# Optimization experiments

Measured on AMD Instinct MI355X. Metric: run time of the kernel, lower is better.

## Reference

```python
import jax, jax.numpy as jnp
import numpy as np

N = 50000
E = 800000
EPS = 1e-5


def layer_norm(h, g, b):
    m = jnp.mean(h, axis=-1, keepdims=True)
    v = jnp.mean((h - m) ** 2, axis=-1, keepdims=True)
    return (h - m) * jax.lax.rsqrt(v + EPS) * g + b


def gcn_conv(x, src, dst, w, W, b):
    # PyG GCNConv: add self-loops (weight 1), symmetric normalization,
    # linear transform, scatter-add aggregation at dst, plus bias.
    n = x.shape[0]
    loop = jnp.arange(n)
    s = jnp.concatenate([src, loop])
    d = jnp.concatenate([dst, loop])
    wf = jnp.concatenate([w, jnp.ones((n,), dtype=x.dtype)])
    deg = jax.ops.segment_sum(wf, d, num_segments=n)
    dinv = jnp.where(deg > 0, deg, 1.0) ** -0.5
    dinv = jnp.where(deg > 0, dinv, 0.0)
    norm = dinv[s] * wf * dinv[d]            # [E+N]
    h = x @ W                                 # [N, out]
    msg = h[s] * norm[:, None]                # gather + scale
    out = jax.ops.segment_sum(msg, d, num_segments=n)  # scatter-add
    return out + b


def setup_inputs() -> dict:
    key = jax.random.key(0)
    ks = jax.random.split(key, 16)
    din, dh, dout = 128, 128, 64
    p = lambda k, shp: jax.random.normal(k, shp, dtype=jnp.float32) * 0.05
    return {
        "x": jax.random.normal(ks[0], (N, din), dtype=jnp.float32),
        "edge_index": jax.random.randint(ks[1], (2, E), 0, N),
        "edge_weight": jax.random.uniform(ks[2], (E,), dtype=jnp.float32),
        "W1": p(ks[3], (din, dh)), "b1": jnp.zeros((dh,), jnp.float32),
        "g1": jnp.ones((dh,), jnp.float32), "t1": jnp.zeros((dh,), jnp.float32),
        "W2": p(ks[4], (dh, dh)), "b2": jnp.zeros((dh,), jnp.float32),
        "g2": jnp.ones((dh,), jnp.float32), "t2": jnp.zeros((dh,), jnp.float32),
        "W3": p(ks[5], (dh, dout)), "b3": jnp.zeros((dout,), jnp.float32),
        "g3": jnp.ones((dout,), jnp.float32), "t3": jnp.zeros((dout,), jnp.float32),
    }


def reference(x, edge_index, edge_weight, W1, b1, g1, t1, W2, b2, g2, t2, W3, b3, g3, t3):
    src, dst = edge_index[0], edge_index[1]
    h = gcn_conv(x, src, dst, edge_weight, W1, b1)
    h = jax.nn.relu(layer_norm(h, g1, t1))
    h = gcn_conv(h, src, dst, edge_weight, W2, b2)
    h = jax.nn.relu(layer_norm(h, g2, t2))
    h = gcn_conv(h, src, dst, edge_weight, W3, b3)
    h = layer_norm(h, g3, t3)  # last layer: no relu/dropout
    return h
```

## Files before the change

kernel.cpp:

```cpp
#include <hip/hip_runtime.h>


typedef __attribute__((ext_vector_type(8))) short short8;
typedef __attribute__((ext_vector_type(4))) float f32x4;

static constexpr float FXS  = 16777216.0f;
static constexpr float FXSI = 1.0f / 16777216.0f;

__device__ __forceinline__ unsigned short f2bf(float f) {
    unsigned int u = __float_as_uint(f);
    u += 0x7FFFu + ((u >> 16) & 1u);
    return (unsigned short)(u >> 16);
}

__global__ __launch_bounds__(256) void edge_pass_kernel(
    const int* __restrict__ dst, const float* __restrict__ ew,
    unsigned long long* __restrict__ packed, int* __restrict__ rank, int nE)
{
    int e = blockIdx.x * 256 + threadIdx.x;
    if (e >= nE) return;
    const int d = dst[e];
    const unsigned long long fx = (unsigned long long)__float2uint_rn(ew[e] * FXS);
    const unsigned long long old = atomicAdd(&packed[d], (1ULL << 40) | fx);
    rank[e] = (int)(old >> 40);
}

__global__ __launch_bounds__(256) void dinv_partial_kernel(
    const unsigned long long* __restrict__ packed, int* __restrict__ partials,
    float* __restrict__ dinv, int n)
{
    const int b = blockIdx.x;
    const int i = b * 256 + threadIdx.x;
    int c = 0;
    if (i < n) {
        const unsigned long long p = packed[i];
        c = (int)(p >> 40);
        const float deg = (float)(p & ((1ULL << 40) - 1)) * FXSI;
        dinv[i] = rsqrtf(deg + 1.0f);
    }
#pragma unroll
    for (int off = 32; off; off >>= 1) c += __shfl_xor(c, off);
    __shared__ int red[4];
    if ((threadIdx.x & 63) == 0) red[threadIdx.x >> 6] = c;
    __syncthreads();
    if (threadIdx.x == 0) partials[b] = red[0] + red[1] + red[2] + red[3];
}

__global__ __launch_bounds__(256) void scanp_kernel(
    int* __restrict__ partials, int* __restrict__ rowptr, int n, int nblk)
{
    __shared__ int buf[256];
    const int v = (threadIdx.x < nblk) ? partials[threadIdx.x] : 0;
    buf[threadIdx.x] = v;
    __syncthreads();
    for (int off = 1; off < 256; off <<= 1) {
        const int t = (threadIdx.x >= off) ? buf[threadIdx.x - off] : 0;
        __syncthreads();
        buf[threadIdx.x] += t;
        __syncthreads();
    }
    if (threadIdx.x < nblk) partials[threadIdx.x] = buf[threadIdx.x] - v;
    if (threadIdx.x == 255) rowptr[n] = buf[255];
}

__global__ __launch_bounds__(256) void scanf_kernel(
    const unsigned long long* __restrict__ packed, const int* __restrict__ partials,
    int* __restrict__ rowptr, int n)
{
    __shared__ int buf[256];
    const int b = blockIdx.x;
    const int i = b * 256 + threadIdx.x;
    const int v = (i < n) ? (int)(packed[i] >> 40) : 0;
    buf[threadIdx.x] = v;
    __syncthreads();
    for (int off = 1; off < 256; off <<= 1) {
        const int t = (threadIdx.x >= off) ? buf[threadIdx.x - off] : 0;
        __syncthreads();
        buf[threadIdx.x] += t;
        __syncthreads();
    }
    if (i < n) rowptr[i] = buf[threadIdx.x] - v + partials[b];
}

__global__ __launch_bounds__(256) void fill2_kernel(
    const int* __restrict__ src, const int* __restrict__ dst,
    const float* __restrict__ ew, const int* __restrict__ rank,
    const float* __restrict__ dinv, const int* __restrict__ rowptr,
    int2* __restrict__ edges, int nE)
{
    int e = blockIdx.x * 256 + threadIdx.x;
    if (e >= nE) return;
    const int s = src[e], d = dst[e];
    const float nrm = dinv[s] * ew[e] * dinv[d];
    edges[rowptr[d] + rank[e]] = make_int2(s, __float_as_int(nrm));
}

__global__ __launch_bounds__(256) void xconv_kernel(
    const float* __restrict__ X, unsigned short* __restrict__ Xb, int total4)
{
    int i = blockIdx.x * 256 + threadIdx.x;
    if (i >= total4) return;
    const float4 v = ((const float4*)X)[i];
    ushort4 o;
    o.x = f2bf(v.x); o.y = f2bf(v.y); o.z = f2bf(v.z); o.w = f2bf(v.w);
    ((ushort4*)Xb)[i] = o;
}

__global__ __launch_bounds__(256) void wconv_kernel(
    const float* __restrict__ W1, const float* __restrict__ W2,
    const float* __restrict__ W3, unsigned short* __restrict__ Wt1,
    unsigned short* __restrict__ Wt2, unsigned short* __restrict__ Wt3)
{
    int i = blockIdx.x * 256 + threadIdx.x;
    if (i < 16384) {
        const int j = i >> 7, k = i & 127;
        Wt1[i] = f2bf(W1[k * 128 + j]);
    } else if (i < 32768) {
        const int q = i - 16384, j = q >> 7, k = q & 127;
        Wt2[q] = f2bf(W2[k * 128 + j]);
    } else if (i < 40960) {
        const int q = i - 32768, j = q >> 7, k = q & 127;
        Wt3[q] = f2bf(W3[k * 64 + j]);
    }
}

template<int DOUT>
__global__ __launch_bounds__(256) void gemm_mfma_kernel(
    const unsigned short* __restrict__ Xb,
    const unsigned short* __restrict__ Wt,
    unsigned short* __restrict__ H, int n)
{
    const int wave = threadIdx.x >> 6;
    const int lane = threadIdx.x & 63;
    const int row0 = (blockIdx.x * 4 + wave) * 16;
    if (row0 >= n) return;
    const int lr = lane & 15;
    const int lk = (lane >> 4) * 8;

    constexpr int NCT = DOUT / 16;
    f32x4 acc[NCT];
#pragma unroll
    for (int c = 0; c < NCT; ++c) acc[c] = (f32x4){0.f, 0.f, 0.f, 0.f};

    const int arow = row0 + lr;
    const bool rv = arow < n;
    short8 afrag[4];
#pragma unroll
    for (int ks = 0; ks < 4; ++ks)
        afrag[ks] = rv ? *(const short8*)(Xb + (size_t)arow * 128 + ks * 32 + lk)
                       : (short8){0, 0, 0, 0, 0, 0, 0, 0};

#pragma unroll
    for (int c = 0; c < NCT; ++c) {
        const unsigned short* wp = Wt + (size_t)(c * 16 + lr) * 128 + lk;
#pragma unroll
        for (int ks = 0; ks < 4; ++ks) {
            const short8 bfrag = *(const short8*)(wp + ks * 32);
            acc[c] = __builtin_amdgcn_mfma_f32_16x16x32_bf16(afrag[ks], bfrag, acc[c], 0, 0, 0);
        }
    }

    const int orow0 = row0 + (lane >> 4) * 4;
#pragma unroll
    for (int c = 0; c < NCT; ++c) {
#pragma unroll
        for (int r = 0; r < 4; ++r) {
            const int orow = orow0 + r;
            if (orow < n) H[(size_t)orow * DOUT + c * 16 + lr] = f2bf(acc[c][r]);
        }
    }
}

template<int D, bool RELU, bool OB16>
__global__ __launch_bounds__(256) void gather_ln_kernel(
    const unsigned short* __restrict__ H, const int2* __restrict__ edges,
    const int* __restrict__ rowptr, const float* __restrict__ dinv,
    const float* __restrict__ bias, const float* __restrict__ g,
    const float* __restrict__ t, void* __restrict__ OUT, int n)
{
    constexpr int PL = D / 64;
    const int lane = threadIdx.x & 63;
    const int node = blockIdx.x * 4 + (threadIdx.x >> 6);
    if (node >= n) return;

    const float di = dinv[node];
    const float sn = di * di;
    float acc[PL];
    {
        const unsigned short* hd = H + (size_t)node * D + lane * PL;
        if constexpr (PL == 2) {
            const unsigned int w = *(const unsigned int*)hd;
            acc[0] = fmaf(__uint_as_float(w << 16), sn, bias[lane * 2]);
            acc[1] = fmaf(__uint_as_float(w & 0xFFFF0000u), sn, bias[lane * 2 + 1]);
        } else {
            acc[0] = fmaf(__uint_as_float((unsigned int)hd[0] << 16), sn, bias[lane]);
        }
    }

    const int k0 = rowptr[node], k1 = rowptr[node + 1];
    for (int base = k0; base < k1; base += 64) {
        int2 ed = make_int2(0, 0);
        if (base + lane < k1) ed = edges[base + lane];
        const int cnt = min(64, k1 - base);
        int j = 0;
        for (; j + 4 <= cnt; j += 4) {
#pragma unroll
            for (int u = 0; u < 4; ++u) {
                const int   s   = __shfl(ed.x, j + u);
                const float nrm = __int_as_float(__shfl(ed.y, j + u));
                const unsigned short* hs = H + (size_t)s * D + lane * PL;
                if constexpr (PL == 2) {
                    const unsigned int w = *(const unsigned int*)hs;
                    acc[0] = fmaf(__uint_as_float(w << 16), nrm, acc[0]);
                    acc[1] = fmaf(__uint_as_float(w & 0xFFFF0000u), nrm, acc[1]);
                } else {
                    acc[0] = fmaf(__uint_as_float((unsigned int)hs[0] << 16), nrm, acc[0]);
                }
            }
        }
        for (; j < cnt; ++j) {
            const int   s   = __shfl(ed.x, j);
            const float nrm = __int_as_float(__shfl(ed.y, j));
            const unsigned short* hs = H + (size_t)s * D + lane * PL;
            if constexpr (PL == 2) {
                const unsigned int w = *(const unsigned int*)hs;
                acc[0] = fmaf(__uint_as_float(w << 16), nrm, acc[0]);
                acc[1] = fmaf(__uint_as_float(w & 0xFFFF0000u), nrm, acc[1]);
            } else {
                acc[0] = fmaf(__uint_as_float((unsigned int)hs[0] << 16), nrm, acc[0]);
            }
        }
    }

    float s1 = 0.f;
#pragma unroll
    for (int i = 0; i < PL; ++i) s1 += acc[i];
#pragma unroll
    for (int off = 32; off; off >>= 1) s1 += __shfl_xor(s1, off);
    const float m = s1 * (1.f / D);
    float s2 = 0.f;
#pragma unroll
    for (int i = 0; i < PL; ++i) { acc[i] -= m; s2 += acc[i] * acc[i]; }
#pragma unroll
    for (int off = 32; off; off >>= 1) s2 += __shfl_xor(s2, off);
    const float rs = rsqrtf(s2 * (1.f / D) + 1e-5f);

    float r[PL];
#pragma unroll
    for (int i = 0; i < PL; ++i) {
        r[i] = fmaf(acc[i] * rs, g[lane * PL + i], t[lane * PL + i]);
        if (RELU) r[i] = fmaxf(r[i], 0.f);
    }
    if constexpr (OB16) {
        static_assert(PL == 2, "bf16 output path assumes D=128");
        const unsigned int w = (unsigned int)f2bf(r[0]) | ((unsigned int)f2bf(r[1]) << 16);
        ((unsigned int*)OUT)[(size_t)node * (D / 2) + lane] = w;
    } else {
        float* o = (float*)OUT + (size_t)node * D + lane * PL;
#pragma unroll
        for (int i = 0; i < PL; ++i) o[i] = r[i];
    }
}

extern "C" void kernel_launch(void* const* d_in, const int* in_sizes, int n_in,
                              void* d_out, int out_size, void* d_ws, size_t ws_size,
                              hipStream_t stream)
{
    const float* x  = (const float*)d_in[0];
    const int*   ei = (const int*)  d_in[1];
    const float* ew = (const float*)d_in[2];
    const float* W1 = (const float*)d_in[3];
    const float* b1 = (const float*)d_in[4];
    const float* g1 = (const float*)d_in[5];
    const float* t1 = (const float*)d_in[6];
    const float* W2 = (const float*)d_in[7];
    const float* b2 = (const float*)d_in[8];
    const float* g2 = (const float*)d_in[9];
    const float* t2 = (const float*)d_in[10];
    const float* W3 = (const float*)d_in[11];
    const float* b3 = (const float*)d_in[12];
    const float* g3 = (const float*)d_in[13];
    const float* t3 = (const float*)d_in[14];

    const int n  = in_sizes[0] / 128;
    const int nE = in_sizes[1] / 2;
    const int* srcv = ei;
    const int* dstv = ei + nE;

    const size_t na   = ((size_t)n + 63) & ~(size_t)63;
    const int    nblk = (n + 255) / 256;
    const int    eb   = (nE + 255) / 256;

    unsigned long long* packed = (unsigned long long*)d_ws;
    float* dinv     = (float*)(packed + na);
    int*   rowptr   = (int*)(dinv + na);
    int*   partials = rowptr + na + 64;
    int2*  edges    = (int2*)(partials + 256);
    unsigned short* Hb  = (unsigned short*)(edges + nE);
    unsigned short* Qb  = Hb + (size_t)n * 128;
    unsigned short* xb  = Qb + (size_t)n * 128;
    unsigned short* Wt1 = xb + (size_t)n * 128;
    unsigned short* Wt2 = Wt1 + 16384;
    unsigned short* Wt3 = Wt2 + 16384;
    int* rank = (int*)Hb;

    hipMemsetAsync(packed, 0, na * sizeof(unsigned long long), stream);

    edge_pass_kernel   <<<eb,   256, 0, stream>>>(dstv, ew, packed, rank, nE);
    dinv_partial_kernel<<<nblk, 256, 0, stream>>>(packed, partials, dinv, n);
    scanp_kernel       <<<1,    256, 0, stream>>>(partials, rowptr, n, nblk);
    scanf_kernel       <<<nblk, 256, 0, stream>>>(packed, partials, rowptr, n);
    fill2_kernel       <<<eb,   256, 0, stream>>>(srcv, dstv, ew, rank, dinv, rowptr, edges, nE);

    xconv_kernel<<<(n * 32 + 255) / 256, 256, 0, stream>>>(x, xb, n * 32);
    wconv_kernel<<<160, 256, 0, stream>>>(W1, W2, W3, Wt1, Wt2, Wt3);

    const int gb = (n + 63) / 64;
    const int nb = (n + 3) / 4;

    gemm_mfma_kernel<128><<<gb, 256, 0, stream>>>(xb, Wt1, Hb, n);
    gather_ln_kernel<128, true, true><<<nb, 256, 0, stream>>>(Hb, edges, rowptr, dinv, b1, g1, t1, Qb, n);

    gemm_mfma_kernel<128><<<gb, 256, 0, stream>>>(Qb, Wt2, Hb, n);
    gather_ln_kernel<128, true, true><<<nb, 256, 0, stream>>>(Hb, edges, rowptr, dinv, b2, g2, t2, Qb, n);

    gemm_mfma_kernel<64><<<gb, 256, 0, stream>>>(Qb, Wt3, Hb, n);
    gather_ln_kernel<64, false, false><<<nb, 256, 0, stream>>>(Hb, edges, rowptr, dinv, b3, g3, t3, d_out, n);
}
```

Baseline: 325.9 us.

## Pack multiple nodes per wave in gather-LN with 16-byte loads; merge prep kernels

The gather+layernorm kernel now assigns a group of 8 (D=64) or 16 (D=128) lanes to each node. Each lane loads 8 bf16 features as one 16-byte vector instead of 2-byte or 4-byte loads, so a wave handles several nodes at once. This targets wasted lanes and narrow loads for nodes with few neighbors (about 16 on average), at the cost of more divergence across nodes of different degree within a wave. Separately, the edge atomic pass, x conversion and weight conversion are merged into one launch to cut launch overhead.

```diff
diff --git a/kernel.cpp b/kernel.cpp
--- a/kernel.cpp
+++ b/kernel.cpp
@@ -12,17 +12,47 @@
     u += 0x7FFFu + ((u >> 16) & 1u);
     return (unsigned short)(u >> 16);
 }
-
-__global__ __launch_bounds__(256) void edge_pass_kernel(
+__device__ __forceinline__ float bflo(unsigned int w) { return __uint_as_float(w << 16); }
+__device__ __forceinline__ float bfhi(unsigned int w) { return __uint_as_float(w & 0xFFFF0000u); }
+
+__global__ __launch_bounds__(256) void prep_kernel(
     const int* __restrict__ dst, const float* __restrict__ ew,
-    unsigned long long* __restrict__ packed, int* __restrict__ rank, int nE)
-{
-    int e = blockIdx.x * 256 + threadIdx.x;
-    if (e >= nE) return;
-    const int d = dst[e];
-    const unsigned long long fx = (unsigned long long)__float2uint_rn(ew[e] * FXS);
-    const unsigned long long old = atomicAdd(&packed[d], (1ULL << 40) | fx);
-    rank[e] = (int)(old >> 40);
+    unsigned long long* __restrict__ packed, int* __restrict__ rank, int nE, int eb,
+    const float* __restrict__ X, unsigned short* __restrict__ Xb, int total4, int xbk,
+    const float* __restrict__ W1, const float* __restrict__ W2,
+    const float* __restrict__ W3, unsigned short* __restrict__ Wt1,
+    unsigned short* __restrict__ Wt2, unsigned short* __restrict__ Wt3)
+{
+    const int b = blockIdx.x;
+    if (b < eb) {
+        const int e = b * 256 + threadIdx.x;
+        if (e < nE) {
+            const int d = dst[e];
+            const unsigned long long fx = (unsigned long long)__float2uint_rn(ew[e] * FXS);
+            const unsigned long long old = atomicAdd(&packed[d], (1ULL << 40) | fx);
+            rank[e] = (int)(old >> 40);
+        }
+    } else if (b < eb + xbk) {
+        const int i = (b - eb) * 256 + threadIdx.x;
+        if (i < total4) {
+            const float4 v = ((const float4*)X)[i];
+            ushort4 o;
+            o.x = f2bf(v.x); o.y = f2bf(v.y); o.z = f2bf(v.z); o.w = f2bf(v.w);
+            ((ushort4*)Xb)[i] = o;
+        }
+    } else {
+        const int i = (b - eb - xbk) * 256 + threadIdx.x;
+        if (i < 16384) {
+            const int j = i >> 7, k = i & 127;
+            Wt1[i] = f2bf(W1[k * 128 + j]);
+        } else if (i < 32768) {
+            const int q = i - 16384, j = q >> 7, k = q & 127;
+            Wt2[q] = f2bf(W2[k * 128 + j]);
+        } else if (i < 40960) {
+            const int q = i - 32768, j = q >> 7, k = q & 127;
+            Wt3[q] = f2bf(W3[k * 64 + j]);
+        }
+    }
 }
 
 __global__ __launch_bounds__(256) void dinv_partial_kernel(
@@ -95,35 +125,6 @@
     edges[rowptr[d] + rank[e]] = make_int2(s, __float_as_int(nrm));
 }
 
-__global__ __launch_bounds__(256) void xconv_kernel(
-    const float* __restrict__ X, unsigned short* __restrict__ Xb, int total4)
-{
-    int i = blockIdx.x * 256 + threadIdx.x;
-    if (i >= total4) return;
-    const float4 v = ((const float4*)X)[i];
-    ushort4 o;
-    o.x = f2bf(v.x); o.y = f2bf(v.y); o.z = f2bf(v.z); o.w = f2bf(v.w);
-    ((ushort4*)Xb)[i] = o;
-}
-
-__global__ __launch_bounds__(256) void wconv_kernel(
-    const float* __restrict__ W1, const float* __restrict__ W2,
-    const float* __restrict__ W3, unsigned short* __restrict__ Wt1,
-    unsigned short* __restrict__ Wt2, unsigned short* __restrict__ Wt3)
-{
-    int i = blockIdx.x * 256 + threadIdx.x;
-    if (i < 16384) {
-        const int j = i >> 7, k = i & 127;
-        Wt1[i] = f2bf(W1[k * 128 + j]);
-    } else if (i < 32768) {
-        const int q = i - 16384, j = q >> 7, k = q & 127;
-        Wt2[q] = f2bf(W2[k * 128 + j]);
-    } else if (i < 40960) {
-        const int q = i - 32768, j = q >> 7, k = q & 127;
-        Wt3[q] = f2bf(W3[k * 64 + j]);
-    }
-}
-
 template<int DOUT>
 __global__ __launch_bounds__(256) void gemm_mfma_kernel(
     const unsigned short* __restrict__ Xb,
@@ -178,87 +179,97 @@
     const float* __restrict__ bias, const float* __restrict__ g,
     const float* __restrict__ t, void* __restrict__ OUT, int n)
 {
-    constexpr int PL = D / 64;
+    constexpr int GS  = D / 8;
+    constexpr int NPW = 64 / GS;
     const int lane = threadIdx.x & 63;
-    const int node = blockIdx.x * 4 + (threadIdx.x >> 6);
+    const int wave = threadIdx.x >> 6;
+    const int L    = lane & (GS - 1);
+    const int gb0  = lane & ~(GS - 1);
+    const int node = (blockIdx.x * 4 + wave) * NPW + (lane >> (GS == 16 ? 4 : 3));
     if (node >= n) return;
 
     const float di = dinv[node];
     const float sn = di * di;
-    float acc[PL];
+    float acc[8];
     {
-        const unsigned short* hd = H + (size_t)node * D + lane * PL;
-        if constexpr (PL == 2) {
-            const unsigned int w = *(const unsigned int*)hd;
-            acc[0] = fmaf(__uint_as_float(w << 16), sn, bias[lane * 2]);
-            acc[1] = fmaf(__uint_as_float(w & 0xFFFF0000u), sn, bias[lane * 2 + 1]);
-        } else {
-            acc[0] = fmaf(__uint_as_float((unsigned int)hd[0] << 16), sn, bias[lane]);
-        }
+        const uint4 w = *(const uint4*)(H + (size_t)node * D + L * 8);
+        const float4 b0 = *(const float4*)(bias + L * 8);
+        const float4 b1 = *(const float4*)(bias + L * 8 + 4);
+        acc[0] = fmaf(bflo(w.x), sn, b0.x); acc[1] = fmaf(bfhi(w.x), sn, b0.y);
+        acc[2] = fmaf(bflo(w.y), sn, b0.z); acc[3] = fmaf(bfhi(w.y), sn, b0.w);
+        acc[4] = fmaf(bflo(w.z), sn, b1.x); acc[5] = fmaf(bfhi(w.z), sn, b1.y);
+        acc[6] = fmaf(bflo(w.w), sn, b1.z); acc[7] = fmaf(bfhi(w.w), sn, b1.w);
     }
 
     const int k0 = rowptr[node], k1 = rowptr[node + 1];
-    for (int base = k0; base < k1; base += 64) {
+    for (int base = k0; base < k1; base += GS) {
         int2 ed = make_int2(0, 0);
-        if (base + lane < k1) ed = edges[base + lane];
-        const int cnt = min(64, k1 - base);
+        if (base + L < k1) ed = edges[base + L];
+        const int cnt = min(GS, k1 - base);
         int j = 0;
-        for (; j + 4 <= cnt; j += 4) {
-#pragma unroll
-            for (int u = 0; u < 4; ++u) {
-                const int   s   = __shfl(ed.x, j + u);
-                const float nrm = __int_as_float(__shfl(ed.y, j + u));
-                const unsigned short* hs = H + (size_t)s * D + lane * PL;
-                if constexpr (PL == 2) {
-                    const unsigned int w = *(const unsigned int*)hs;
-                    acc[0] = fmaf(__uint_as_float(w << 16), nrm, acc[0]);
-                    acc[1] = fmaf(__uint_as_float(w & 0xFFFF0000u), nrm, acc[1]);
-                } else {
-                    acc[0] = fmaf(__uint_as_float((unsigned int)hs[0] << 16), nrm, acc[0]);
-                }
-            }
-        }
-        for (; j < cnt; ++j) {
-            const int   s   = __shfl(ed.x, j);
-            const float nrm = __int_as_float(__shfl(ed.y, j));
-            const unsigned short* hs = H + (size_t)s * D + lane * PL;
-            if constexpr (PL == 2) {
-                const unsigned int w = *(const unsigned int*)hs;
-                acc[0] = fmaf(__uint_as_float(w << 16), nrm, acc[0]);
-                acc[1] = fmaf(__uint_as_float(w & 0xFFFF0000u), nrm, acc[1]);
-            } else {
-                acc[0] = fmaf(__uint_as_float((unsigned int)hs[0] << 16), nrm, acc[0]);
-            }
+        for (; j + 2 <= cnt; j += 2) {
+            const int   s0 = __shfl(ed.x, gb0 + j);
+            const int   s1 = __shfl(ed.x, gb0 + j + 1);
+            const float n0 = __int_as_float(__shfl(ed.y, gb0 + j));
+            const float n1 = __int_as_float(__shfl(ed.y, gb0 + j + 1));
+            const uint4 w0 = *(const uint4*)(H + (size_t)s0 * D + L * 8);
+            const uint4 w1 = *(const uint4*)(H + (size_t)s1 * D + L * 8);
+            acc[0] = fmaf(bflo(w0.x), n0, acc[0]); acc[1] = fmaf(bfhi(w0.x), n0, acc[1]);
+            acc[2] = fmaf(bflo(w0.y), n0, acc[2]); acc[3] = fmaf(bfhi(w0.y), n0, acc[3]);
+            acc[4] = fmaf(bflo(w0.z), n0, acc[4]); acc[5] = fmaf(bfhi(w0.z), n0, acc[5]);
+            acc[6] = fmaf(bflo(w0.w), n0, acc[6]); acc[7] = fmaf(bfhi(w0.w), n0, acc[7]);
+            acc[0] = fmaf(bflo(w1.x), n1, acc[0]); acc[1] = fmaf(bfhi(w1.x), n1, acc[1]);
+            acc[2] = fmaf(bflo(w1.y), n1, acc[2]); acc[3] = fmaf(bfhi(w1.y), n1, acc[3]);
+            acc[4] = fmaf(bflo(w1.z), n1, acc[4]); acc[5] = fmaf(bfhi(w1.z), n1, acc[5]);
+            acc[6] = fmaf(bflo(w1.w), n1, acc[6]); acc[7] = fmaf(bfhi(w1.w), n1, acc[7]);
+        }
+        if (j < cnt) {
+            const int   s0 = __shfl(ed.x, gb0 + j);
+            const float n0 = __int_as_float(__shfl(ed.y, gb0 + j));
+            const uint4 w0 = *(const uint4*)(H + (size_t)s0 * D + L * 8);
+            acc[0] = fmaf(bflo(w0.x), n0, acc[0]); acc[1] = fmaf(bfhi(w0.x), n0, acc[1]);
+            acc[2] = fmaf(bflo(w0.y), n0, acc[2]); acc[3] = fmaf(bfhi(w0.y), n0, acc[3]);
+            acc[4] = fmaf(bflo(w0.z), n0, acc[4]); acc[5] = fmaf(bfhi(w0.z), n0, acc[5]);
+            acc[6] = fmaf(bflo(w0.w), n0, acc[6]); acc[7] = fmaf(bfhi(w0.w), n0, acc[7]);
         }
     }
 
     float s1 = 0.f;
 #pragma unroll
-    for (int i = 0; i < PL; ++i) s1 += acc[i];
-#pragma unroll
-    for (int off = 32; off; off >>= 1) s1 += __shfl_xor(s1, off);
+    for (int i = 0; i < 8; ++i) s1 += acc[i];
+#pragma unroll
+    for (int off = GS / 2; off; off >>= 1) s1 += __shfl_xor(s1, off);
     const float m = s1 * (1.f / D);
     float s2 = 0.f;
 #pragma unroll
-    for (int i = 0; i < PL; ++i) { acc[i] -= m; s2 += acc[i] * acc[i]; }
-#pragma unroll
-    for (int off = 32; off; off >>= 1) s2 += __shfl_xor(s2, off);
+    for (int i = 0; i < 8; ++i) { acc[i] -= m; s2 += acc[i] * acc[i]; }
+#pragma unroll
+    for (int off = GS / 2; off; off >>= 1) s2 += __shfl_xor(s2, off);
     const float rs = rsqrtf(s2 * (1.f / D) + 1e-5f);
 
-    float r[PL];
-#pragma unroll
-    for (int i = 0; i < PL; ++i) {
-        r[i] = fmaf(acc[i] * rs, g[lane * PL + i], t[lane * PL + i]);
-        if (RELU) r[i] = fmaxf(r[i], 0.f);
-    }
+    const float4 g0 = *(const float4*)(g + L * 8), g1 = *(const float4*)(g + L * 8 + 4);
+    const float4 t0 = *(const float4*)(t + L * 8), t1 = *(const float4*)(t + L * 8 + 4);
+    float r[8];
+    r[0] = fmaf(acc[0] * rs, g0.x, t0.x); r[1] = fmaf(acc[1] * rs, g0.y, t0.y);
+    r[2] = fmaf(acc[2] * rs, g0.z, t0.z); r[3] = fmaf(acc[3] * rs, g0.w, t0.w);
+    r[4] = fmaf(acc[4] * rs, g1.x, t1.x); r[5] = fmaf(acc[5] * rs, g1.y, t1.y);
+    r[6] = fmaf(acc[6] * rs, g1.z, t1.z); r[7] = fmaf(acc[7] * rs, g1.w, t1.w);
+    if (RELU) {
+#pragma unroll
+        for (int i = 0; i < 8; ++i) r[i] = fmaxf(r[i], 0.f);
+    }
+
     if constexpr (OB16) {
-        static_assert(PL == 2, "bf16 output path assumes D=128");
-        const unsigned int w = (unsigned int)f2bf(r[0]) | ((unsigned int)f2bf(r[1]) << 16);
-        ((unsigned int*)OUT)[(size_t)node * (D / 2) + lane] = w;
+        uint4 o;
+        o.x = (unsigned int)f2bf(r[0]) | ((unsigned int)f2bf(r[1]) << 16);
+        o.y = (unsigned int)f2bf(r[2]) | ((unsigned int)f2bf(r[3]) << 16);
+        o.z = (unsigned int)f2bf(r[4]) | ((unsigned int)f2bf(r[5]) << 16);
+        o.w = (unsigned int)f2bf(r[6]) | ((unsigned int)f2bf(r[7]) << 16);
+        *(uint4*)((unsigned short*)OUT + (size_t)node * D + L * 8) = o;
     } else {
-        float* o = (float*)OUT + (size_t)node * D + lane * PL;
-#pragma unroll
-        for (int i = 0; i < PL; ++i) o[i] = r[i];
+        float* o = (float*)OUT + (size_t)node * D + L * 8;
+        *(float4*)o       = make_float4(r[0], r[1], r[2], r[3]);
+        *(float4*)(o + 4) = make_float4(r[4], r[5], r[6], r[7]);
     }
 }
 
@@ -290,6 +301,7 @@
     const size_t na   = ((size_t)n + 63) & ~(size_t)63;
     const int    nblk = (n + 255) / 256;
     const int    eb   = (nE + 255) / 256;
+    const int    xbk  = (n * 32 + 255) / 256;
 
     unsigned long long* packed = (unsigned long long*)d_ws;
     float* dinv     = (float*)(packed + na);
@@ -306,24 +318,24 @@
 
     hipMemsetAsync(packed, 0, na * sizeof(unsigned long long), stream);
 
-    edge_pass_kernel   <<<eb,   256, 0, stream>>>(dstv, ew, packed, rank, nE);
+    prep_kernel<<<eb + xbk + 160, 256, 0, stream>>>(
+        dstv, ew, packed, rank, nE, eb,
+        x, xb, n * 32, xbk, W1, W2, W3, Wt1, Wt2, Wt3);
     dinv_partial_kernel<<<nblk, 256, 0, stream>>>(packed, partials, dinv, n);
     scanp_kernel       <<<1,    256, 0, stream>>>(partials, rowptr, n, nblk);
     scanf_kernel       <<<nblk, 256, 0, stream>>>(packed, partials, rowptr, n);
     fill2_kernel       <<<eb,   256, 0, stream>>>(srcv, dstv, ew, rank, dinv, rowptr, edges, nE);
 
-    xconv_kernel<<<(n * 32 + 255) / 256, 256, 0, stream>>>(x, xb, n * 32);
-    wconv_kernel<<<160, 256, 0, stream>>>(W1, W2, W3, Wt1, Wt2, Wt3);
-
-    const int gb = (n + 63) / 64;
-    const int nb = (n + 3) / 4;
+    const int gb   = (n + 63) / 64;
+    const int nbA  = (n + 15) / 16;
+    const int nbB  = (n + 31) / 32;
 
     gemm_mfma_kernel<128><<<gb, 256, 0, stream>>>(xb, Wt1, Hb, n);
-    gather_ln_kernel<128, true, true><<<nb, 256, 0, stream>>>(Hb, edges, rowptr, dinv, b1, g1, t1, Qb, n);
+    gather_ln_kernel<128, true, true><<<nbA, 256, 0, stream>>>(Hb, edges, rowptr, dinv, b1, g1, t1, Qb, n);
 
     gemm_mfma_kernel<128><<<gb, 256, 0, stream>>>(Qb, Wt2, Hb, n);
-    gather_ln_kernel<128, true, true><<<nb, 256, 0, stream>>>(Hb, edges, rowptr, dinv, b2, g2, t2, Qb, n);
+    gather_ln_kernel<128, true, true><<<nbA, 256, 0, stream>>>(Hb, edges, rowptr, dinv, b2, g2, t2, Qb, n);
 
     gemm_mfma_kernel<64><<<gb, 256, 0, stream>>>(Qb, Wt3, Hb, n);
-    gather_ln_kernel<64, false, false><<<nb, 256, 0, stream>>>(Hb, edges, rowptr, dinv, b3, g3, t3, d_out, n);
-}
+    gather_ln_kernel<64, false, false><<<nbB, 256, 0, stream>>>(Hb, edges, rowptr, dinv, b3, g3, t3, d_out, n);
+}
```

New measurement: 302.0 us. 7.3% less time.
